# Kernel optimization log

Measured on AMD Instinct MI355X. Metric: run time of the kernel, lower is better.

The kernel has to match this reference:

```python
import jax, jax.numpy as jnp
import numpy as np

BLOCK = 64       # _aether_cfg['block_size']
JL_DIM = 32      # epsilon_jl_bridge d_out
EPS_GOV = 0.5    # fixed governor eps (governor.target)
ROPE_BASE = 10000.0
RMS_EPS = 1e-6


def _normalize(x, axis=-1):
    n = jnp.sqrt(jnp.sum(x * x, axis=axis, keepdims=True))
    return x / jnp.maximum(n, 1e-12)


def _rms_norm(x):
    return x * jax.lax.rsqrt(jnp.mean(x * x, axis=-1, keepdims=True) + RMS_EPS)


def _rope(x, cos, sin):
    half = x.shape[-1] // 2
    x1, x2 = x[..., :half], x[..., half:]
    return jnp.concatenate([x1 * cos + x2 * sin, -x1 * sin + x2 * cos], axis=-1)


def setup_inputs() -> dict:
    key = jax.random.key(0)
    ks = jax.random.split(key, 6)
    B, S, Dm, H = 2, 2048, 2048, 16
    sc = 1.0 / np.sqrt(Dm)
    x = jax.random.normal(ks[0], (B, S, Dm), jnp.float32)
    Wq = jax.random.normal(ks[1], (Dm, Dm), jnp.float32) * sc
    Wk = jax.random.normal(ks[2], (Dm, Dm), jnp.float32) * sc
    Wv = jax.random.normal(ks[3], (Dm, Dm), jnp.float32) * sc
    Wo = jax.random.normal(ks[4], (Dm, Dm), jnp.float32) * sc
    q_gain = jnp.ones((H,), jnp.float32)
    return {"x": x, "Wq": Wq, "Wk": Wk, "Wv": Wv, "Wo": Wo, "q_gain": q_gain}


def reference(x, Wq, Wk, Wv, Wo, q_gain):
    B, S, Dm = x.shape
    H = q_gain.shape[0]
    Dh = Dm // H

    # QKV projections (bias-free linear, torch weight layout [out,in])
    q = (x @ Wq.T).reshape(B, S, H, Dh).transpose(0, 2, 1, 3)  # (B,H,S,Dh)
    k = (x @ Wk.T).reshape(B, S, H, Dh).transpose(0, 2, 1, 3)
    v = (x @ Wv.T).reshape(B, S, H, Dh).transpose(0, 2, 1, 3)

    # RoPE tables
    inv_freq = 1.0 / (ROPE_BASE ** (jnp.arange(0, Dh, 2, dtype=jnp.float32) / Dh))
    freqs = jnp.outer(jnp.arange(S, dtype=jnp.float32), inv_freq)  # (S,Dh/2)
    cos = jnp.cos(freqs)[None, None]
    sin = jnp.sin(freqs)[None, None]

    q = _rope(_rms_norm(q), cos, sin) * q_gain[None, :, None, None]
    k = _rope(_rms_norm(k), cos, sin)

    # --- aether sparse SDPA: JL block bounds -> top-k blocks -> gather -> SDPA ---
    N = S // BLOCK  # number of KV blocks (static)
    proj = jax.random.normal(jax.random.key(42), (Dh, JL_DIM), jnp.float32) / np.sqrt(JL_DIM)

    q_proj = _normalize(q.mean(axis=2, keepdims=True) @ proj)          # (B,H,1,JL)
    k_blocks = k.reshape(B, H, N, BLOCK, Dh)
    k_proj = _normalize(k_blocks @ proj)                               # (B,H,N,BLOCK,JL)
    centroids = _normalize(k_proj.mean(axis=3))                        # (B,H,N,JL)
    radii = jnp.clip(
        1.0 - jnp.min(jnp.sum(k_proj * centroids[:, :, :, None, :], axis=-1), axis=-1),
        0.0, 1.0)                                                      # (B,H,N)
    ub = jnp.einsum('bhqj,bhnj->bhqn', q_proj, centroids) + radii[:, :, None, :]
    scores = ub[:, :, 0, :]                                            # (B,H,N)
    # force-include the last two blocks (union in the original code)
    scores = scores.at[:, :, N - 2:].set(jnp.inf)

    n_keep = max(2, int(N * min(1.0, EPS_GOV))) + 2                    # static
    _, top_idx = jax.lax.top_k(scores, n_keep)                         # (B,H,n_keep)
    top_idx = jnp.sort(top_idx, axis=-1)
    idx = (top_idx[..., None] * BLOCK + jnp.arange(BLOCK)).reshape(B, H, -1)  # (B,H,K)

    k_s = jnp.take_along_axis(k, idx[..., None], axis=2)               # (B,H,K,Dh)
    v_s = jnp.take_along_axis(v, idx[..., None], axis=2)

    att = jax.nn.softmax(
        jnp.einsum('bhqd,bhkd->bhqk', q, k_s) / np.sqrt(Dh), axis=-1)  # (B,H,S,K)
    y = jnp.einsum('bhqk,bhkd->bhqd', att, v_s)                        # (B,H,S,Dh)

    y = y.transpose(0, 2, 1, 3).reshape(B, S, Dm)
    return y @ Wo.T
```

## Files before the change

### kernel.cpp

```cpp
#include <hip/hip_runtime.h>
#include <hip/hip_bf16.h>

#define B_ 2
#define S_ 2048
#define DM 2048
#define H_ 16
#define DH 128
#define NBLK 32
#define NKEEP 18
#define BH (B_ * H_)

typedef __attribute__((ext_vector_type(8))) short short8;
typedef __attribute__((ext_vector_type(8))) _Float16 f16x8;
typedef __attribute__((ext_vector_type(4))) _Float16 f16x4;
typedef __attribute__((ext_vector_type(4))) float f32x4;

#define GLOAD16(gp, lp)                                                        \
  __builtin_amdgcn_global_load_lds(                                            \
      (const __attribute__((address_space(1))) unsigned int*)(const void*)(gp),\
      (__attribute__((address_space(3))) unsigned int*)(void*)(lp), 16, 0, 0)

__device__ __forceinline__ unsigned short f32_to_bf16(float f) {
  unsigned u = __float_as_uint(f);
  unsigned r = (u + 0x7fffu + ((u >> 16) & 1u)) >> 16;
  return (unsigned short)r;
}
__device__ __forceinline__ float bf16_to_f32(unsigned short h) {
  return __uint_as_float(((unsigned)h) << 16);
}

__device__ __forceinline__ unsigned rotl32(unsigned x, int r) {
  return (x << r) | (x >> (32 - r));
}

__device__ __forceinline__ float erfinv_f32(float x) {
  float w = -log1pf(-x * x);
  float p;
  if (w < 5.0f) {
    w -= 2.5f;
    p = 2.81022636e-08f;
    p = fmaf(p, w, 3.43273939e-07f);
    p = fmaf(p, w, -3.5233877e-06f);
    p = fmaf(p, w, -4.39150654e-06f);
    p = fmaf(p, w, 0.00021858087f);
    p = fmaf(p, w, -0.00125372503f);
    p = fmaf(p, w, -0.00417768164f);
    p = fmaf(p, w, 0.246640727f);
    p = fmaf(p, w, 1.50140941f);
  } else {
    w = sqrtf(w) - 3.0f;
    p = -0.000200214257f;
    p = fmaf(p, w, 0.000100950558f);
    p = fmaf(p, w, 0.00134934322f);
    p = fmaf(p, w, -0.00367342844f);
    p = fmaf(p, w, 0.00573950773f);
    p = fmaf(p, w, -0.0076224613f);
    p = fmaf(p, w, 0.00943887047f);
    p = fmaf(p, w, 1.00167406f);
    p = fmaf(p, w, 2.83297682f);
  }
  return p * x;
}

__device__ __forceinline__ float bits_to_normal(unsigned b) {
  float f = __uint_as_float((b >> 9) | 0x3f800000u) - 1.0f;
  const float lo = -0.9999999403953552f;
  float u = fmaxf(lo, fmaf(f, 2.0f, lo));
  return 1.4142135623730951f * erfinv_f32(u);
}

__global__ void proj_kernel(float* __restrict__ proj) {
  int i = blockIdx.x * blockDim.x + threadIdx.x;
  if (i >= 4096) return;
  unsigned k0 = 0u, k1 = 42u;
  unsigned k2 = 0x1BD11BDAu ^ k0 ^ k1;
  unsigned x0 = 0u, x1 = (unsigned)i;
  x0 += k0; x1 += k1;
#define QR(r) { x0 += x1; x1 = rotl32(x1, r); x1 ^= x0; }
  QR(13) QR(15) QR(26) QR(6)   x0 += k1; x1 += k2 + 1u;
  QR(17) QR(29) QR(16) QR(24)  x0 += k2; x1 += k0 + 2u;
  QR(13) QR(15) QR(26) QR(6)   x0 += k0; x1 += k1 + 3u;
  QR(17) QR(29) QR(16) QR(24)  x0 += k1; x1 += k2 + 4u;
  QR(13) QR(15) QR(26) QR(6)   x0 += k2; x1 += k0 + 5u;
#undef QR
  proj[i] = bits_to_normal(x0 ^ x1) / 5.656854249492381f;
}

__global__ void rope_table_kernel(float* __restrict__ cosb, float* __restrict__ sinb) {
  int s = blockIdx.x;
  int j = threadIdx.x;
  double e = (double)(2 * j) / 128.0;
  double invf = 1.0 / pow(10000.0, e);
  float freq = (float)s * (float)invf;
  cosb[s * 64 + j] = (float)cos((double)freq);
  sinb[s * 64 + j] = (float)sin((double)freq);
}

__global__ __launch_bounds__(256) void split_x3_kernel(const float* __restrict__ in,
                                                       unsigned short* __restrict__ hi,
                                                       unsigned short* __restrict__ lo,
                                                       _Float16* __restrict__ f16,
                                                       int n4) {
  int i = blockIdx.x * blockDim.x + threadIdx.x;
  if (i >= n4) return;
  float4 v = ((const float4*)in)[i];
  ushort4 hv, lv;
  f16x4 fv;
  hv.x = f32_to_bf16(v.x); lv.x = f32_to_bf16(v.x - bf16_to_f32(hv.x)); fv[0] = (_Float16)v.x;
  hv.y = f32_to_bf16(v.y); lv.y = f32_to_bf16(v.y - bf16_to_f32(hv.y)); fv[1] = (_Float16)v.y;
  hv.z = f32_to_bf16(v.z); lv.z = f32_to_bf16(v.z - bf16_to_f32(hv.z)); fv[2] = (_Float16)v.z;
  hv.w = f32_to_bf16(v.w); lv.w = f32_to_bf16(v.w - bf16_to_f32(hv.w)); fv[3] = (_Float16)v.w;
  ((ushort4*)hi)[i] = hv;
  ((ushort4*)lo)[i] = lv;
  ((f16x4*)f16)[i] = fv;
}

__global__ __launch_bounds__(256) void split_kernel(const float* __restrict__ in,
                                                    unsigned short* __restrict__ hi,
                                                    unsigned short* __restrict__ lo,
                                                    int n4) {
  int i = blockIdx.x * blockDim.x + threadIdx.x;
  if (i >= n4) return;
  float4 v = ((const float4*)in)[i];
  ushort4 hv, lv;
  hv.x = f32_to_bf16(v.x); lv.x = f32_to_bf16(v.x - bf16_to_f32(hv.x));
  hv.y = f32_to_bf16(v.y); lv.y = f32_to_bf16(v.y - bf16_to_f32(hv.y));
  hv.z = f32_to_bf16(v.z); lv.z = f32_to_bf16(v.z - bf16_to_f32(hv.z));
  hv.w = f32_to_bf16(v.w); lv.w = f32_to_bf16(v.w - bf16_to_f32(hv.w));
  ((ushort4*)hi)[i] = hv;
  ((ushort4*)lo)[i] = lv;
}

__global__ __launch_bounds__(256) void split_f16_kernel(const float* __restrict__ in,
                                                        _Float16* __restrict__ f16,
                                                        int n4) {
  int i = blockIdx.x * blockDim.x + threadIdx.x;
  if (i >= n4) return;
  float4 v = ((const float4*)in)[i];
  f16x4 fv;
  fv[0] = (_Float16)v.x; fv[1] = (_Float16)v.y;
  fv[2] = (_Float16)v.z; fv[3] = (_Float16)v.w;
  ((f16x4*)f16)[i] = fv;
}

__global__ __launch_bounds__(256) void mfma_gemm_k(const unsigned short* __restrict__ Ahi,
                                                   const unsigned short* __restrict__ Alo,
                                                   const unsigned short* __restrict__ Whi,
                                                   const unsigned short* __restrict__ Wlo,
                                                   float* __restrict__ C) {
  __shared__ char smem[65536];
  const int t = threadIdx.x, l = t & 63, w = t >> 6;
  const int lin = blockIdx.y * gridDim.x + blockIdx.x;
  const int cpx = (gridDim.x * gridDim.y) >> 3;
  const int swz = (lin & 7) * cpx + (lin >> 3);
  const int n0 = (swz % gridDim.x) * 128;
  const int m0 = (swz / gridDim.x) * 128;
  const int wm = w >> 1, wn = w & 1;
  const int lrow = l & 15;
  const int lk8 = (l >> 4) * 8;

  const unsigned short* gAh = Ahi + (size_t)(m0 + 32 * w + lrow) * DM + lk8;
  const unsigned short* gAl = Alo + (size_t)(m0 + 32 * w + lrow) * DM + lk8;
  const unsigned short* gBh = Whi + (size_t)(n0 + 32 * w + lrow) * DM + lk8;
  const unsigned short* gBl = Wlo + (size_t)(n0 + 32 * w + lrow) * DM + lk8;

  auto STAGE = [&](int k0, int c) {
    char* lA = smem + c * 32768 + w * 2048;
    GLOAD16(gAh + k0, lA);
    GLOAD16(gAh + 16 * DM + k0, lA + 1024);
    GLOAD16(gAl + k0, lA + 8192);
    GLOAD16(gAl + 16 * DM + k0, lA + 8192 + 1024);
    GLOAD16(gBh + k0, lA + 16384);
    GLOAD16(gBh + 16 * DM + k0, lA + 16384 + 1024);
    GLOAD16(gBl + k0, lA + 24576);
    GLOAD16(gBl + 16 * DM + k0, lA + 24576 + 1024);
  };

  f32x4 acc[4][4];
#pragma unroll
  for (int i = 0; i < 4; ++i)
#pragma unroll
    for (int j = 0; j < 4; ++j) acc[i][j] = (f32x4){0.f, 0.f, 0.f, 0.f};

  STAGE(0, 0);
  int cur = 0;

  for (int k0 = 0; k0 < DM; k0 += 32) {
    if (k0 + 32 < DM) {
      STAGE(k0 + 32, cur ^ 1);
      asm volatile("s_waitcnt vmcnt(8)" ::: "memory");
    } else {
      asm volatile("s_waitcnt vmcnt(0)" ::: "memory");
    }
    __builtin_amdgcn_s_barrier();

    char* buf = smem + cur * 32768;
    short8 ah[4], al[4], bh[4], bl[4];
#pragma unroll
    for (int f = 0; f < 4; ++f) {
      ah[f] = *(const short8*)(buf + (wm * 4 + f) * 1024 + l * 16);
      al[f] = *(const short8*)(buf + 8192 + (wm * 4 + f) * 1024 + l * 16);
      bh[f] = *(const short8*)(buf + 16384 + (wn * 4 + f) * 1024 + l * 16);
      bl[f] = *(const short8*)(buf + 24576 + (wn * 4 + f) * 1024 + l * 16);
    }
    __builtin_amdgcn_s_setprio(1);
#pragma unroll
    for (int i = 0; i < 4; ++i)
#pragma unroll
      for (int j = 0; j < 4; ++j) {
        acc[i][j] = __builtin_amdgcn_mfma_f32_16x16x32_bf16(ah[i], bh[j], acc[i][j], 0, 0, 0);
        acc[i][j] = __builtin_amdgcn_mfma_f32_16x16x32_bf16(ah[i], bl[j], acc[i][j], 0, 0, 0);
        acc[i][j] = __builtin_amdgcn_mfma_f32_16x16x32_bf16(al[i], bh[j], acc[i][j], 0, 0, 0);
      }
    __builtin_amdgcn_s_setprio(0);
    __builtin_amdgcn_s_barrier();
    cur ^= 1;
  }

#pragma unroll
  for (int i = 0; i < 4; ++i) {
    int row0 = m0 + wm * 64 + i * 16 + (l >> 4) * 4;
#pragma unroll
    for (int j = 0; j < 4; ++j) {
      int col = n0 + wn * 64 + j * 16 + (l & 15);
      int h = col >> 7, d = col & 127;
#pragma unroll
      for (int r = 0; r < 4; ++r) {
        int mm = row0 + r;
        int b = mm >> 11, s = mm & (S_ - 1);
        C[(((size_t)(b * H_ + h) * S_) + s) * DH + d] = acc[i][j][r];
      }
    }
  }
}

__global__ __launch_bounds__(512, 2) void mfma_gemm_qv(const _Float16* __restrict__ A,
                                                       const _Float16* __restrict__ W,
                                                       float* __restrict__ Cq,
                                                       _Float16* __restrict__ vt) {
  __shared__ char smem[65536];
  const int t = threadIdx.x, l = t & 63, w = t >> 6;
  const int lin = blockIdx.y * gridDim.x + blockIdx.x;
  const int swz = (lin & 7) * 32 + (lin >> 3);
  const int n0 = (swz & 15) * 256;
  const int m0 = (swz >> 4) * 256;
  const int wm = w >> 2, wn = w & 3;
  const int lr = l & 15;
  const int lg8 = (l >> 4) * 8;
  const size_t rstep = (size_t)16 * DM;

  const _Float16* gA = A + (size_t)(m0 + w * 32 + lr) * DM + lg8;
  const _Float16* gB = W + (size_t)(n0 + w * 32 + lr) * DM + lg8;

  auto STAGE = [&](int k0, int c) {
    char* base = smem + c * 32768 + w * 2048;
    GLOAD16(gA + k0, base);
    GLOAD16(gA + rstep + k0, base + 1024);
    GLOAD16(gB + k0, base + 16384);
    GLOAD16(gB + rstep + k0, base + 16384 + 1024);
  };

  f32x4 acc[8][4];
#pragma unroll
  for (int i = 0; i < 8; ++i)
#pragma unroll
    for (int j = 0; j < 4; ++j) acc[i][j] = (f32x4){0.f, 0.f, 0.f, 0.f};

  STAGE(0, 0);
  int cur = 0;

  for (int k0 = 0; k0 < DM; k0 += 32) {
    if (k0 + 32 < DM) {
      STAGE(k0 + 32, cur ^ 1);
      asm volatile("s_waitcnt vmcnt(4)" ::: "memory");
    } else {
      asm volatile("s_waitcnt vmcnt(0)" ::: "memory");
    }
    __builtin_amdgcn_s_barrier();

    char* buf = smem + cur * 32768;
    f16x8 b[4];
#pragma unroll
    for (int j = 0; j < 4; ++j)
      b[j] = *(const f16x8*)(buf + 16384 + (wn * 4 + j) * 1024 + l * 16);
    __builtin_amdgcn_s_setprio(1);
#pragma unroll
    for (int i = 0; i < 8; ++i) {
      f16x8 a = *(const f16x8*)(buf + (wm * 8 + i) * 1024 + l * 16);
#pragma unroll
      for (int j = 0; j < 4; ++j)
        acc[i][j] = __builtin_amdgcn_mfma_f32_16x16x32_f16(a, b[j], acc[i][j], 0, 0, 0);
    }
    __builtin_amdgcn_s_setprio(0);
    __builtin_amdgcn_s_barrier();
    cur ^= 1;
  }

#pragma unroll
  for (int m = 0; m < 8; ++m) {
    int row0 = m0 + wm * 128 + m * 16 + (l >> 4) * 4;
#pragma unroll
    for (int n = 0; n < 4; ++n) {
      int col = n0 + wn * 64 + n * 16 + (l & 15);
      if (col < DM) {
        int h = col >> 7, d = col & 127;
#pragma unroll
        for (int r = 0; r < 4; ++r) {
          int mm = row0 + r;
          int b2 = mm >> 11, s = mm & (S_ - 1);
          Cq[(((size_t)(b2 * H_ + h) * S_) + s) * DH + d] = acc[m][n][r];
        }
      } else {
        int vcol = col - DM;
        int h = vcol >> 7, d = vcol & 127;
        int b2 = row0 >> 11, s0 = row0 & (S_ - 1);
        f16x4 vv;
        vv[0] = (_Float16)acc[m][n][0];
        vv[1] = (_Float16)acc[m][n][1];
        vv[2] = (_Float16)acc[m][n][2];
        vv[3] = (_Float16)acc[m][n][3];
        *(f16x4*)(vt + (((size_t)(b2 * H_ + h)) * DH + d) * S_ + s0) = vv;
      }
    }
  }
}

template <int MODE>
__global__ __launch_bounds__(256) void mfma_gemm_f16(const _Float16* __restrict__ A,
                                                     const _Float16* __restrict__ W,
                                                     void* __restrict__ Cout) {
  __shared__ char smem[65536];
  const int t = threadIdx.x, l = t & 63, w = t >> 6;
  const int lin = blockIdx.y * gridDim.x + blockIdx.x;
  const int cpx = (gridDim.x * gridDim.y) >> 3;
  const int swz = (lin & 7) * cpx + (lin >> 3);
  const int n0 = (swz % gridDim.x) * 128;
  const int m0 = (swz / gridDim.x) * 128;
  const int wm = w >> 1, wn = w & 1;
  const int lr = l & 15;
  const int lg8 = (l >> 4) * 8;

  auto STAGE = [&](int k0, int c) {
    char* base = smem + c * 32768;
#pragma unroll
    for (int f0 = 0; f0 < 4; ++f0) {
      int f = w * 4 + f0;
      int rb = f >> 1, kh = f & 1;
      GLOAD16(A + (size_t)(m0 + rb * 16 + lr) * DM + k0 + kh * 32 + lg8,
              base + f * 1024);
      GLOAD16(W + (size_t)(n0 + rb * 16 + lr) * DM + k0 + kh * 32 + lg8,
              base + 16384 + f * 1024);
    }
  };

  f32x4 acc[4][4];
#pragma unroll
  for (int i = 0; i < 4; ++i)
#pragma unroll
    for (int j = 0; j < 4; ++j) acc[i][j] = (f32x4){0.f, 0.f, 0.f, 0.f};

  STAGE(0, 0);
  int cur = 0;

  for (int k0 = 0; k0 < DM; k0 += 64) {
    if (k0 + 64 < DM) {
      STAGE(k0 + 64, cur ^ 1);
      asm volatile("s_waitcnt vmcnt(8)" ::: "memory");
    } else {
      asm volatile("s_waitcnt vmcnt(0)" ::: "memory");
    }
    __builtin_amdgcn_s_barrier();

    char* buf = smem + cur * 32768;
    f16x8 a[4][2], b[4][2];
#pragma unroll
    for (int i = 0; i < 4; ++i)
#pragma unroll
      for (int kh = 0; kh < 2; ++kh) {
        a[i][kh] = *(const f16x8*)(buf + ((wm * 4 + i) * 2 + kh) * 1024 + l * 16);
        b[i][kh] = *(const f16x8*)(buf + 16384 + ((wn * 4 + i) * 2 + kh) * 1024 + l * 16);
      }
    __builtin_amdgcn_s_setprio(1);
#pragma unroll
    for (int i = 0; i < 4; ++i)
#pragma unroll
      for (int j = 0; j < 4; ++j) {
        acc[i][j] = __builtin_amdgcn_mfma_f32_16x16x32_f16(a[i][0], b[j][0], acc[i][j], 0, 0, 0);
        acc[i][j] = __builtin_amdgcn_mfma_f32_16x16x32_f16(a[i][1], b[j][1], acc[i][j], 0, 0, 0);
      }
    __builtin_amdgcn_s_setprio(0);
    __builtin_amdgcn_s_barrier();
    cur ^= 1;
  }

#pragma unroll
  for (int i = 0; i < 4; ++i) {
    int row0 = m0 + wm * 64 + i * 16 + (l >> 4) * 4;
#pragma unroll
    for (int j = 0; j < 4; ++j) {
      int col = n0 + wn * 64 + j * 16 + (l & 15);
      if constexpr (MODE == 1) {
        float* C = (float*)Cout;
#pragma unroll
        for (int r = 0; r < 4; ++r)
          C[(size_t)(row0 + r) * DM + col] = acc[i][j][r];
      }
    }
  }
}

__global__ __launch_bounds__(256) void rmsrope_kernel(float* __restrict__ q,
                                                      float* __restrict__ k,
                                                      _Float16* __restrict__ kf,
                                                      const float* __restrict__ cosb,
                                                      const float* __restrict__ sinb,
                                                      const float* __restrict__ qg) {
  int w = threadIdx.x >> 6;
  int lane = threadIdx.x & 63;
  long row = (long)blockIdx.x * 4 + w;
  bool isq = row < (long)BH * S_;
  float* base = isq ? q : k;
  long r = isq ? row : row - (long)BH * S_;
  float* p = base + r * DH;
  int s = (int)(r & (S_ - 1));
  int h = (int)((r >> 11) & (H_ - 1));
  float x1 = p[lane], x2 = p[lane + 64];
  float ss = fmaf(x1, x1, x2 * x2);
#pragma unroll
  for (int off = 32; off; off >>= 1) ss += __shfl_xor(ss, off);
  float rms = rsqrtf(ss * (1.0f / 128.0f) + 1e-6f);
  float n1 = x1 * rms, n2 = x2 * rms;
  float c = cosb[s * 64 + lane], sn = sinb[s * 64 + lane];
  float o1 = fmaf(n1, c, n2 * sn);
  float o2 = fmaf(-n1, sn, n2 * c);
  if (isq) { float g = qg[h]; o1 *= g; o2 *= g; }
  p[lane] = o1;
  p[lane + 64] = o2;
  if (!isq) {
    kf[r * DH + lane] = (_Float16)o1;
    kf[r * DH + lane + 64] = (_Float16)o2;
  }
}

__global__ __launch_bounds__(256) void qmean_part_kernel(const float* __restrict__ q,
                                                         float* __restrict__ partial) {
  __shared__ float red[256];
  const int bh = blockIdx.x >> 4, chunk = blockIdx.x & 15;
  const int t = threadIdx.x;
  const int d = t & 127, half = t >> 7;
  const float* qb = q + ((size_t)bh * S_ + chunk * 128 + half * 64) * DH;
  float sum = 0.0f;
#pragma unroll 4
  for (int s = 0; s < 64; ++s) sum += qb[(size_t)s * DH + d];
  red[t] = sum;
  __syncthreads();
  if (t < 128) partial[(size_t)blockIdx.x * 128 + t] = red[t] + red[t + 128];
}

__global__ void qproj_kernel(const float* __restrict__ partial,
                             const float* __restrict__ proj,
                             float* __restrict__ qp) {
  __shared__ float meanq[128];
  __shared__ float qps[32];
  __shared__ float nrm;
  const int bh = blockIdx.x, t = threadIdx.x;
  float s = 0.0f;
#pragma unroll
  for (int c = 0; c < 16; ++c) s += partial[((size_t)bh * 16 + c) * 128 + t];
  meanq[t] = s * (1.0f / 2048.0f);
  __syncthreads();
  if (t < 32) {
    float sum = 0.0f;
    for (int d = 0; d < 128; ++d) sum = fmaf(meanq[d], proj[d * 32 + t], sum);
    qps[t] = sum;
  }
  __syncthreads();
  if (t == 0) {
    float sum = 0.0f;
    for (int j = 0; j < 32; ++j) sum += qps[j] * qps[j];
    nrm = 1.0f / fmaxf(sqrtf(sum), 1e-12f);
  }
  __syncthreads();
  if (t < 32) qp[bh * 32 + t] = qps[t] * nrm;
}

__global__ __launch_bounds__(256) void kscore_kernel(const float* __restrict__ k,
                                                     const float* __restrict__ proj,
                                                     const float* __restrict__ qp,
                                                     float* __restrict__ scores) {
  __shared__ float ps[128][32];
  __shared__ float kp[64][33];
  __shared__ float cent[33];
  __shared__ float nrm;
  const int bh = blockIdx.x >> 5, n = blockIdx.x & 31;
  const int t = threadIdx.x;
  for (int i = t; i < 4096; i += 256) ps[i >> 5][i & 31] = proj[i];
  const float* kn = k + ((size_t)bh * S_ + n * 64) * DH;
  __syncthreads();
  {
    int row = t >> 2, j0 = (t & 3) * 8;
    float accv[8];
#pragma unroll
    for (int jj = 0; jj < 8; ++jj) accv[jj] = 0.0f;
#pragma unroll 4
    for (int d = 0; d < 128; ++d) {
      float kv = kn[(size_t)row * DH + d];
#pragma unroll
      for (int jj = 0; jj < 8; ++jj) accv[jj] = fmaf(kv, ps[d][j0 + jj], accv[jj]);
    }
#pragma unroll
    for (int jj = 0; jj < 8; ++jj) kp[row][j0 + jj] = accv[jj];
  }
  __syncthreads();
  if (t < 64) {
    float sum = 0.0f;
    for (int j = 0; j < 32; ++j) sum += kp[t][j] * kp[t][j];
    float scl = 1.0f / fmaxf(sqrtf(sum), 1e-12f);
    for (int j = 0; j < 32; ++j) kp[t][j] *= scl;
  }
  __syncthreads();
  if (t < 32) {
    float sum = 0.0f;
    for (int r2 = 0; r2 < 64; ++r2) sum += kp[r2][t];
    cent[t] = sum * (1.0f / 64.0f);
  }
  __syncthreads();
  if (t == 0) {
    float sum = 0.0f;
    for (int j = 0; j < 32; ++j) sum += cent[j] * cent[j];
    nrm = 1.0f / fmaxf(sqrtf(sum), 1e-12f);
  }
  __syncthreads();
  if (t < 32) cent[t] *= nrm;
  __syncthreads();
  if (t < 64) {
    float dt = 0.0f;
    for (int j = 0; j < 32; ++j) dt = fmaf(kp[t][j], cent[j], dt);
#pragma unroll
    for (int off = 32; off; off >>= 1) dt = fminf(dt, __shfl_xor(dt, off));
    if (t == 0) {
      float radius = fminf(fmaxf(1.0f - dt, 0.0f), 1.0f);
      float dq = 0.0f;
      for (int j = 0; j < 32; ++j) dq = fmaf(qp[bh * 32 + j], cent[j], dq);
      scores[bh * 32 + n] = dq + radius;
    }
  }
}

__global__ void topk_kernel(const float* __restrict__ scores, int* __restrict__ top_idx) {
  if (threadIdx.x != 0) return;
  const int bh = blockIdx.x;
  float sc[NBLK];
  for (int j = 0; j < NBLK; ++j) sc[j] = scores[bh * 32 + j];
  sc[NBLK - 2] = INFINITY;
  sc[NBLK - 1] = INFINITY;
  int chosen[NKEEP];
  bool used[NBLK];
  for (int j = 0; j < NBLK; ++j) used[j] = false;
  for (int kk = 0; kk < NKEEP; ++kk) {
    int best = -1;
    float bv = 0.0f;
    for (int j = 0; j < NBLK; ++j)
      if (!used[j] && (best < 0 || sc[j] > bv)) { bv = sc[j]; best = j; }
    used[best] = true;
    chosen[kk] = best;
  }
  for (int a = 1; a < NKEEP; ++a) {
    int v2 = chosen[a], b2 = a - 1;
    while (b2 >= 0 && chosen[b2] > v2) { chosen[b2 + 1] = chosen[b2]; --b2; }
    chosen[b2 + 1] = v2;
  }
  for (int a = 0; a < NKEEP; ++a) top_idx[bh * NKEEP + a] = chosen[a];
}

__global__ __launch_bounds__(256) void attn_mfma_kernel(const float* __restrict__ q,
                                                        const _Float16* __restrict__ kf,
                                                        const _Float16* __restrict__ vt,
                                                        const int* __restrict__ top_idx,
                                                        _Float16* __restrict__ yf) {
  __shared__ char lds[74752];
  const int bh = blockIdx.x >> 5;
  const int qt = blockIdx.x & 31;
  const int t = threadIdx.x, l = t & 63, w = t >> 6;
  const int lr = l & 15, lg = l >> 4;
  const float scale = 0.08838834764831843f;

  f16x8 qf[4];
  {
    const float* qbase = q + ((size_t)(bh * S_ + qt * 64 + w * 16 + lr)) * DH + lg * 8;
#pragma unroll
    for (int dc = 0; dc < 4; ++dc) {
      float4 v0 = *(const float4*)(qbase + dc * 32);
      float4 v1 = *(const float4*)(qbase + dc * 32 + 4);
      f16x8 h;
      h[0] = (_Float16)v0.x; h[1] = (_Float16)v0.y; h[2] = (_Float16)v0.z; h[3] = (_Float16)v0.w;
      h[4] = (_Float16)v1.x; h[5] = (_Float16)v1.y; h[6] = (_Float16)v1.z; h[7] = (_Float16)v1.w;
      qf[dc] = h;
    }
  }

  float m_[4] = {-INFINITY, -INFINITY, -INFINITY, -INFINITY};
  float ls[4] = {0.f, 0.f, 0.f, 0.f};
  f32x4 yacc[8];
#pragma unroll
  for (int dt = 0; dt < 8; ++dt) yacc[dt] = (f32x4){0.f, 0.f, 0.f, 0.f};

  char* Pw = lds + 65536 + w * 2304;

  const _Float16* kb0 = kf + (size_t)bh * S_ * DH;
  const _Float16* vb0 = vt + (size_t)bh * DH * S_;
  const int* idxp = top_idx + bh * NKEEP;

  auto STAGE = [&](int blk, int c) {
    char* base = lds + c * 32768;
#pragma unroll
    for (int f0 = 0; f0 < 4; ++f0) {
      int f = w * 4 + f0;
      int kt = f >> 2, dc = f & 3;
      GLOAD16(kb0 + (size_t)(blk * 64 + kt * 16 + lr) * DH + dc * 32 + lg * 8,
              base + f * 1024);
      int K0 = f >> 3, dt = f & 7;
      GLOAD16(vb0 + (size_t)(dt * 16 + lr) * S_ + blk * 64 + K0 * 32 + lg * 8,
              base + 16384 + f * 1024);
    }
  };

  int cur = 0;
  STAGE(idxp[0], 0);

  for (int it = 0; it < NKEEP; ++it) {
    if (it + 1 < NKEEP) {
      STAGE(idxp[it + 1], cur ^ 1);
      asm volatile("s_waitcnt vmcnt(8)" ::: "memory");
    } else {
      asm volatile("s_waitcnt vmcnt(0)" ::: "memory");
    }
    __builtin_amdgcn_s_barrier();
    char* buf = lds + cur * 32768;

    f32x4 sacc[4];
#pragma unroll
    for (int kt = 0; kt < 4; ++kt) sacc[kt] = (f32x4){0.f, 0.f, 0.f, 0.f};
    __builtin_amdgcn_s_setprio(1);
#pragma unroll
    for (int kt = 0; kt < 4; ++kt)
#pragma unroll
      for (int dc = 0; dc < 4; ++dc) {
        f16x8 kfr = *(const f16x8*)(buf + (kt * 4 + dc) * 1024 + l * 16);
        sacc[kt] = __builtin_amdgcn_mfma_f32_16x16x32_f16(qf[dc], kfr, sacc[kt], 0, 0, 0);
      }
    __builtin_amdgcn_s_setprio(0);

    float p[4][4];
#pragma unroll
    for (int r = 0; r < 4; ++r) {
      float mt = fmaxf(fmaxf(sacc[0][r], sacc[1][r]), fmaxf(sacc[2][r], sacc[3][r])) * scale;
#pragma unroll
      for (int off = 1; off < 16; off <<= 1) mt = fmaxf(mt, __shfl_xor(mt, off));
      float mn = fmaxf(m_[r], mt);
      float corr = __expf(m_[r] - mn);
      float rs = 0.f;
#pragma unroll
      for (int kt = 0; kt < 4; ++kt) {
        p[kt][r] = __expf(fmaf(sacc[kt][r], scale, -mn));
        rs += p[kt][r];
      }
#pragma unroll
      for (int off = 1; off < 16; off <<= 1) rs += __shfl_xor(rs, off);
      ls[r] = ls[r] * corr + rs;
      m_[r] = mn;
#pragma unroll
      for (int dt = 0; dt < 8; ++dt) yacc[dt][r] *= corr;
    }

#pragma unroll
    for (int kt = 0; kt < 4; ++kt)
#pragma unroll
      for (int r = 0; r < 4; ++r)
        *(_Float16*)(Pw + (lg * 4 + r) * 144 + (kt * 16 + lr) * 2) = (_Float16)p[kt][r];

    __builtin_amdgcn_s_setprio(1);
#pragma unroll
    for (int K0 = 0; K0 < 2; ++K0) {
      f16x8 pa = *(const f16x8*)(Pw + lr * 144 + K0 * 64 + lg * 16);
#pragma unroll
      for (int dt = 0; dt < 8; ++dt) {
        f16x8 vf = *(const f16x8*)(buf + 16384 + (K0 * 8 + dt) * 1024 + l * 16);
        yacc[dt] = __builtin_amdgcn_mfma_f32_16x16x32_f16(pa, vf, yacc[dt], 0, 0, 0);
      }
    }
    __builtin_amdgcn_s_setprio(0);

    __builtin_amdgcn_s_barrier();
    cur ^= 1;
  }

  const int b = bh >> 4, h = bh & (H_ - 1);
  float inv[4];
#pragma unroll
  for (int r = 0; r < 4; ++r) inv[r] = 1.0f / ls[r];
#pragma unroll
  for (int r = 0; r < 4; ++r) {
    int srow = qt * 64 + w * 16 + lg * 4 + r;
    size_t off0 = ((size_t)b * S_ + srow) * DM + h * DH + lr;
#pragma unroll
    for (int dt = 0; dt < 8; ++dt)
      yf[off0 + dt * 16] = (_Float16)(yacc[dt][r] * inv[r]);
  }
}

extern "C" void kernel_launch(void* const* d_in, const int* in_sizes, int n_in,
                              void* d_out, int out_size, void* d_ws, size_t ws_size,
                              hipStream_t stream) {
  const float* x  = (const float*)d_in[0];
  const float* Wq = (const float*)d_in[1];
  const float* Wk = (const float*)d_in[2];
  const float* Wv = (const float*)d_in[3];
  const float* Wo = (const float*)d_in[4];
  const float* qg = (const float*)d_in[5];
  float* out = (float*)d_out;

  const size_t NE = (size_t)BH * S_ * DH;
  const size_t WE = (size_t)DM * DM;
  char* p = (char*)d_ws;
  float* q_ws = (float*)p; p += NE * 4;
  float* k_ws = (float*)p; p += NE * 4;
  unsigned short* xhi = (unsigned short*)p; p += NE * 2;
  unsigned short* xlo = (unsigned short*)p; p += NE * 2;
  _Float16* xf16 = (_Float16*)p; p += NE * 2;
  unsigned short* wkhi = (unsigned short*)p; p += WE * 2;
  unsigned short* wklo = (unsigned short*)p; p += WE * 2;
  _Float16* wqv = (_Float16*)p; p += 2 * WE * 2;
  float* cosb = (float*)p; p += (size_t)S_ * 64 * 4;
  float* sinb = (float*)p; p += (size_t)S_ * 64 * 4;
  float* projb = (float*)p; p += 4096 * 4;
  int* idxb = (int*)p; p += BH * NKEEP * 4;
  float* scores = (float*)p; p += BH * NBLK * 4;
  float* qpbuf = (float*)p; p += BH * 32 * 4;
  float* qpart = cosb;
  _Float16* vt = (_Float16*)xlo;
  _Float16* kf16 = (_Float16*)xf16;
  _Float16* yf16 = (_Float16*)xhi;
  _Float16* wo = wqv;

  const int nx4 = (int)(NE / 4);
  const int nw4 = (int)(WE / 4);

  proj_kernel<<<dim3(16), dim3(256), 0, stream>>>(projb);
  rope_table_kernel<<<dim3(S_), dim3(64), 0, stream>>>(cosb, sinb);
  split_x3_kernel<<<dim3(nx4 / 256), dim3(256), 0, stream>>>(x, xhi, xlo, xf16, nx4);
  split_kernel<<<dim3(nw4 / 256), dim3(256), 0, stream>>>(Wk, wkhi, wklo, nw4);
  split_f16_kernel<<<dim3(nw4 / 256), dim3(256), 0, stream>>>(Wq, wqv, nw4);
  split_f16_kernel<<<dim3(nw4 / 256), dim3(256), 0, stream>>>(Wv, wqv + WE, nw4);

  mfma_gemm_k<<<dim3(16, 32), dim3(256), 0, stream>>>(xhi, xlo, wkhi, wklo, k_ws);

  mfma_gemm_qv<<<dim3(16, 16), dim3(512), 0, stream>>>(xf16, wqv, q_ws, vt);

  rmsrope_kernel<<<dim3((2 * BH * S_) / 4), dim3(256), 0, stream>>>(q_ws, k_ws, kf16, cosb, sinb, qg);

  qmean_part_kernel<<<dim3(BH * 16), dim3(256), 0, stream>>>(q_ws, qpart);
  qproj_kernel<<<dim3(BH), dim3(128), 0, stream>>>(qpart, projb, qpbuf);
  kscore_kernel<<<dim3(BH * NBLK), dim3(256), 0, stream>>>(k_ws, projb, qpbuf, scores);
  topk_kernel<<<dim3(BH), dim3(64), 0, stream>>>(scores, idxb);

  attn_mfma_kernel<<<dim3(BH * 32), dim3(256), 0, stream>>>(q_ws, kf16, vt, idxb, yf16);

  split_f16_kernel<<<dim3(nw4 / 256), dim3(256), 0, stream>>>(Wo, wo, nw4);
  mfma_gemm_f16<1><<<dim3(16, 32), dim3(256), 0, stream>>>(yf16, wo, out);
}
```

Baseline: 476.2 us.

## Split-K the K projection GEMM with 256x256 tiles and fuse partial sum into rmsrope

The K projection GEMM (bf16 hi/lo split, three MFMAs per tile) moves from 128x128 tiles with 256 threads to 256x256 tiles with 512 threads, using split-K into two halves. The partial sums are written to two buffers and added inside a new K-only rms/rope kernel. The goal is more data reuse per tile while keeping enough blocks (256) to fill the GPU. The cost is an extra fp32 partial buffer round trip, and fp16 K now lives in the wkhi buffer. The q rms/rope runs as a separate kernel.

```diff
diff --git a/kernel.cpp b/kernel.cpp
--- a/kernel.cpp
+++ b/kernel.cpp
@@ -143,50 +143,55 @@
   ((f16x4*)f16)[i] = fv;
 }
 
-__global__ __launch_bounds__(256) void mfma_gemm_k(const unsigned short* __restrict__ Ahi,
-                                                   const unsigned short* __restrict__ Alo,
-                                                   const unsigned short* __restrict__ Whi,
-                                                   const unsigned short* __restrict__ Wlo,
-                                                   float* __restrict__ C) {
-  __shared__ char smem[65536];
+__global__ __launch_bounds__(512, 2) void mfma_gemm_k_sk(const unsigned short* __restrict__ Ahi,
+                                                         const unsigned short* __restrict__ Alo,
+                                                         const unsigned short* __restrict__ Whi,
+                                                         const unsigned short* __restrict__ Wlo,
+                                                         float* __restrict__ kp0,
+                                                         float* __restrict__ kp1) {
+  __shared__ char smem[131072];
   const int t = threadIdx.x, l = t & 63, w = t >> 6;
-  const int lin = blockIdx.y * gridDim.x + blockIdx.x;
-  const int cpx = (gridDim.x * gridDim.y) >> 3;
-  const int swz = (lin & 7) * cpx + (lin >> 3);
-  const int n0 = (swz % gridDim.x) * 128;
-  const int m0 = (swz / gridDim.x) * 128;
-  const int wm = w >> 1, wn = w & 1;
-  const int lrow = l & 15;
-  const int lk8 = (l >> 4) * 8;
-
-  const unsigned short* gAh = Ahi + (size_t)(m0 + 32 * w + lrow) * DM + lk8;
-  const unsigned short* gAl = Alo + (size_t)(m0 + 32 * w + lrow) * DM + lk8;
-  const unsigned short* gBh = Whi + (size_t)(n0 + 32 * w + lrow) * DM + lk8;
-  const unsigned short* gBl = Wlo + (size_t)(n0 + 32 * w + lrow) * DM + lk8;
+  const int lin = blockIdx.z * 128 + blockIdx.y * 8 + blockIdx.x;
+  const int swz = (lin & 7) * 32 + (lin >> 3);
+  const int kz = swz >> 7;
+  const int idx = swz & 127;
+  const int n0 = (idx & 7) * 256;
+  const int m0 = (idx >> 3) * 256;
+  const int kbase = kz * 1024;
+  float* C = kz ? kp1 : kp0;
+  const int wm = w >> 2, wn = w & 3;
+  const int lr = l & 15;
+  const int lg8 = (l >> 4) * 8;
+  const size_t rstep = (size_t)16 * DM;
+
+  const unsigned short* gAh = Ahi + (size_t)(m0 + w * 32 + lr) * DM + lg8;
+  const unsigned short* gAl = Alo + (size_t)(m0 + w * 32 + lr) * DM + lg8;
+  const unsigned short* gBh = Whi + (size_t)(n0 + w * 32 + lr) * DM + lg8;
+  const unsigned short* gBl = Wlo + (size_t)(n0 + w * 32 + lr) * DM + lg8;
 
   auto STAGE = [&](int k0, int c) {
-    char* lA = smem + c * 32768 + w * 2048;
-    GLOAD16(gAh + k0, lA);
-    GLOAD16(gAh + 16 * DM + k0, lA + 1024);
-    GLOAD16(gAl + k0, lA + 8192);
-    GLOAD16(gAl + 16 * DM + k0, lA + 8192 + 1024);
-    GLOAD16(gBh + k0, lA + 16384);
-    GLOAD16(gBh + 16 * DM + k0, lA + 16384 + 1024);
-    GLOAD16(gBl + k0, lA + 24576);
-    GLOAD16(gBl + 16 * DM + k0, lA + 24576 + 1024);
+    char* base = smem + c * 65536 + w * 2048;
+    GLOAD16(gAh + k0, base);
+    GLOAD16(gAh + rstep + k0, base + 1024);
+    GLOAD16(gAl + k0, base + 16384);
+    GLOAD16(gAl + rstep + k0, base + 16384 + 1024);
+    GLOAD16(gBh + k0, base + 32768);
+    GLOAD16(gBh + rstep + k0, base + 32768 + 1024);
+    GLOAD16(gBl + k0, base + 49152);
+    GLOAD16(gBl + rstep + k0, base + 49152 + 1024);
   };
 
-  f32x4 acc[4][4];
-#pragma unroll
-  for (int i = 0; i < 4; ++i)
+  f32x4 acc[8][4];
+#pragma unroll
+  for (int i = 0; i < 8; ++i)
 #pragma unroll
     for (int j = 0; j < 4; ++j) acc[i][j] = (f32x4){0.f, 0.f, 0.f, 0.f};
 
-  STAGE(0, 0);
+  STAGE(kbase, 0);
   int cur = 0;
 
-  for (int k0 = 0; k0 < DM; k0 += 32) {
-    if (k0 + 32 < DM) {
+  for (int k0 = kbase; k0 < kbase + 1024; k0 += 32) {
+    if (k0 + 32 < kbase + 1024) {
       STAGE(k0 + 32, cur ^ 1);
       asm volatile("s_waitcnt vmcnt(8)" ::: "memory");
     } else {
@@ -194,41 +199,50 @@
     }
     __builtin_amdgcn_s_barrier();
 
-    char* buf = smem + cur * 32768;
-    short8 ah[4], al[4], bh[4], bl[4];
+    char* buf = smem + cur * 65536;
+    short8 bh[4], bl[4];
 #pragma unroll
     for (int f = 0; f < 4; ++f) {
-      ah[f] = *(const short8*)(buf + (wm * 4 + f) * 1024 + l * 16);
-      al[f] = *(const short8*)(buf + 8192 + (wm * 4 + f) * 1024 + l * 16);
-      bh[f] = *(const short8*)(buf + 16384 + (wn * 4 + f) * 1024 + l * 16);
-      bl[f] = *(const short8*)(buf + 24576 + (wn * 4 + f) * 1024 + l * 16);
+      bh[f] = *(const short8*)(buf + 32768 + (wn * 4 + f) * 1024 + l * 16);
+      bl[f] = *(const short8*)(buf + 49152 + (wn * 4 + f) * 1024 + l * 16);
     }
     __builtin_amdgcn_s_setprio(1);
 #pragma unroll
-    for (int i = 0; i < 4; ++i)
-#pragma unroll
-      for (int j = 0; j < 4; ++j) {
-        acc[i][j] = __builtin_amdgcn_mfma_f32_16x16x32_bf16(ah[i], bh[j], acc[i][j], 0, 0, 0);
-        acc[i][j] = __builtin_amdgcn_mfma_f32_16x16x32_bf16(ah[i], bl[j], acc[i][j], 0, 0, 0);
-        acc[i][j] = __builtin_amdgcn_mfma_f32_16x16x32_bf16(al[i], bh[j], acc[i][j], 0, 0, 0);
-      }
+    for (int mp = 0; mp < 4; ++mp) {
+      short8 ah0 = *(const short8*)(buf + (wm * 8 + 2 * mp) * 1024 + l * 16);
+      short8 ah1 = *(const short8*)(buf + (wm * 8 + 2 * mp + 1) * 1024 + l * 16);
+      short8 al0 = *(const short8*)(buf + 16384 + (wm * 8 + 2 * mp) * 1024 + l * 16);
+      short8 al1 = *(const short8*)(buf + 16384 + (wm * 8 + 2 * mp + 1) * 1024 + l * 16);
+#pragma unroll
+      for (int n = 0; n < 4; ++n) {
+        acc[2 * mp][n] = __builtin_amdgcn_mfma_f32_16x16x32_bf16(ah0, bh[n], acc[2 * mp][n], 0, 0, 0);
+        acc[2 * mp][n] = __builtin_amdgcn_mfma_f32_16x16x32_bf16(ah0, bl[n], acc[2 * mp][n], 0, 0, 0);
+        acc[2 * mp][n] = __builtin_amdgcn_mfma_f32_16x16x32_bf16(al0, bh[n], acc[2 * mp][n], 0, 0, 0);
+      }
+#pragma unroll
+      for (int n = 0; n < 4; ++n) {
+        acc[2 * mp + 1][n] = __builtin_amdgcn_mfma_f32_16x16x32_bf16(ah1, bh[n], acc[2 * mp + 1][n], 0, 0, 0);
+        acc[2 * mp + 1][n] = __builtin_amdgcn_mfma_f32_16x16x32_bf16(ah1, bl[n], acc[2 * mp + 1][n], 0, 0, 0);
+        acc[2 * mp + 1][n] = __builtin_amdgcn_mfma_f32_16x16x32_bf16(al1, bh[n], acc[2 * mp + 1][n], 0, 0, 0);
+      }
+    }
     __builtin_amdgcn_s_setprio(0);
     __builtin_amdgcn_s_barrier();
     cur ^= 1;
   }
 
 #pragma unroll
-  for (int i = 0; i < 4; ++i) {
-    int row0 = m0 + wm * 64 + i * 16 + (l >> 4) * 4;
-#pragma unroll
-    for (int j = 0; j < 4; ++j) {
-      int col = n0 + wn * 64 + j * 16 + (l & 15);
+  for (int m = 0; m < 8; ++m) {
+    int row0 = m0 + wm * 128 + m * 16 + (l >> 4) * 4;
+#pragma unroll
+    for (int n = 0; n < 4; ++n) {
+      int col = n0 + wn * 64 + n * 16 + (l & 15);
       int h = col >> 7, d = col & 127;
 #pragma unroll
       for (int r = 0; r < 4; ++r) {
         int mm = row0 + r;
         int b = mm >> 11, s = mm & (S_ - 1);
-        C[(((size_t)(b * H_ + h) * S_) + s) * DH + d] = acc[i][j][r];
+        C[(((size_t)(b * H_ + h) * S_) + s) * DH + d] = acc[m][n][r];
       }
     }
   }
@@ -409,22 +423,19 @@
   }
 }
 
-__global__ __launch_bounds__(256) void rmsrope_kernel(float* __restrict__ q,
-                                                      float* __restrict__ k,
-                                                      _Float16* __restrict__ kf,
-                                                      const float* __restrict__ cosb,
-                                                      const float* __restrict__ sinb,
-                                                      const float* __restrict__ qg) {
+__global__ __launch_bounds__(256) void rmsrope_k_kernel(float* __restrict__ k,
+                                                        const float* __restrict__ kp1,
+                                                        _Float16* __restrict__ kf,
+                                                        const float* __restrict__ cosb,
+                                                        const float* __restrict__ sinb) {
   int w = threadIdx.x >> 6;
   int lane = threadIdx.x & 63;
-  long row = (long)blockIdx.x * 4 + w;
-  bool isq = row < (long)BH * S_;
-  float* base = isq ? q : k;
-  long r = isq ? row : row - (long)BH * S_;
-  float* p = base + r * DH;
+  long r = (long)blockIdx.x * 4 + w;
+  float* p = k + r * DH;
+  const float* p1 = kp1 + r * DH;
   int s = (int)(r & (S_ - 1));
-  int h = (int)((r >> 11) & (H_ - 1));
-  float x1 = p[lane], x2 = p[lane + 64];
+  float x1 = p[lane] + p1[lane];
+  float x2 = p[lane + 64] + p1[lane + 64];
   float ss = fmaf(x1, x1, x2 * x2);
 #pragma unroll
   for (int off = 32; off; off >>= 1) ss += __shfl_xor(ss, off);
@@ -433,13 +444,34 @@
   float c = cosb[s * 64 + lane], sn = sinb[s * 64 + lane];
   float o1 = fmaf(n1, c, n2 * sn);
   float o2 = fmaf(-n1, sn, n2 * c);
-  if (isq) { float g = qg[h]; o1 *= g; o2 *= g; }
   p[lane] = o1;
   p[lane + 64] = o2;
-  if (!isq) {
-    kf[r * DH + lane] = (_Float16)o1;
-    kf[r * DH + lane + 64] = (_Float16)o2;
-  }
+  kf[r * DH + lane] = (_Float16)o1;
+  kf[r * DH + lane + 64] = (_Float16)o2;
+}
+
+__global__ __launch_bounds__(256) void rmsrope_q_kernel(float* __restrict__ q,
+                                                        const float* __restrict__ cosb,
+                                                        const float* __restrict__ sinb,
+                                                        const float* __restrict__ qg) {
+  int w = threadIdx.x >> 6;
+  int lane = threadIdx.x & 63;
+  long r = (long)blockIdx.x * 4 + w;
+  float* p = q + r * DH;
+  int s = (int)(r & (S_ - 1));
+  int h = (int)((r >> 11) & (H_ - 1));
+  float x1 = p[lane], x2 = p[lane + 64];
+  float ss = fmaf(x1, x1, x2 * x2);
+#pragma unroll
+  for (int off = 32; off; off >>= 1) ss += __shfl_xor(ss, off);
+  float rms = rsqrtf(ss * (1.0f / 128.0f) + 1e-6f);
+  float n1 = x1 * rms, n2 = x2 * rms;
+  float c = cosb[s * 64 + lane], sn = sinb[s * 64 + lane];
+  float g = qg[h];
+  float o1 = fmaf(n1, c, n2 * sn) * g;
+  float o2 = fmaf(-n1, sn, n2 * c) * g;
+  p[lane] = o1;
+  p[lane + 64] = o2;
 }
 
 __global__ __launch_bounds__(256) void qmean_part_kernel(const float* __restrict__ q,
@@ -738,8 +770,9 @@
   float* scores = (float*)p; p += BH * NBLK * 4;
   float* qpbuf = (float*)p; p += BH * 32 * 4;
   float* qpart = cosb;
+  float* kpart1 = q_ws;
+  _Float16* kf16 = (_Float16*)wkhi;
   _Float16* vt = (_Float16*)xlo;
-  _Float16* kf16 = (_Float16*)xf16;
   _Float16* yf16 = (_Float16*)xhi;
   _Float16* wo = wqv;
 
@@ -753,11 +786,14 @@
   split_f16_kernel<<<dim3(nw4 / 256), dim3(256), 0, stream>>>(Wq, wqv, nw4);
   split_f16_kernel<<<dim3(nw4 / 256), dim3(256), 0, stream>>>(Wv, wqv + WE, nw4);
 
-  mfma_gemm_k<<<dim3(16, 32), dim3(256), 0, stream>>>(xhi, xlo, wkhi, wklo, k_ws);
+  mfma_gemm_k_sk<<<dim3(8, 16, 2), dim3(512), 0, stream>>>(xhi, xlo, wkhi, wklo,
+                                                           k_ws, kpart1);
+
+  rmsrope_k_kernel<<<dim3((BH * S_) / 4), dim3(256), 0, stream>>>(k_ws, kpart1, kf16, cosb, sinb);
 
   mfma_gemm_qv<<<dim3(16, 16), dim3(512), 0, stream>>>(xf16, wqv, q_ws, vt);
 
-  rmsrope_kernel<<<dim3((2 * BH * S_) / 4), dim3(256), 0, stream>>>(q_ws, k_ws, kf16, cosb, sinb, qg);
+  rmsrope_q_kernel<<<dim3((BH * S_) / 4), dim3(256), 0, stream>>>(q_ws, cosb, sinb, qg);
 
   qmean_part_kernel<<<dim3(BH * 16), dim3(256), 0, stream>>>(q_ws, qpart);
   qproj_kernel<<<dim3(BH), dim3(128), 0, stream>>>(qpart, projb, qpbuf);
```

Result: faster. 463.3 us (-2.7%).
